# Kernel optimization log

Hardware: AMD Instinct MI355X
Metric: run time of the kernel (lower is better)

The kernel has to match this reference:

```python
import jax, jax.numpy as jnp
import numpy as np
from jax import lax

B, H, W, T = 4, 480, 640, 32
FRAME_PERIOD_US = 10000.0


def setup_inputs() -> dict:
    key = jax.random.key(0)
    k1, k2, k3 = jax.random.split(key, 3)
    # log-intensity frames, (H, W, B*T), frames of each video contiguous
    log_images = 0.25 * jax.random.normal(k1, (H, W, B * T), dtype=jnp.float32)
    video_len = jnp.full((B,), T, dtype=jnp.int64)
    image_ts = jnp.broadcast_to(jnp.arange(T, dtype=jnp.float32) * FRAME_PERIOD_US, (B, T))
    first_times = jnp.ones((B,), dtype=jnp.float32)
    # per-pixel contrast thresholds: N(mu=0.1, std=0.022), clamped to [0.01, 1.0]
    thresholds = jnp.clip(jax.random.normal(k2, (2, B, H, W), dtype=jnp.float32) * 0.022 + 0.1, 0.01, 1.0)
    log_states = jnp.zeros((B, H, W), dtype=jnp.float32)
    timestamps = jnp.zeros((B, H, W), dtype=jnp.float32)
    prev_image_ts = jnp.zeros((B,), dtype=jnp.float32)
    refractory_periods = jnp.full((B,), 100.0, dtype=jnp.float32)  # us
    leak_rates = jnp.full((B,), 0.1e-6, dtype=jnp.float32)   # per us
    shot_rates = jnp.full((B,), 1.0e-6, dtype=jnp.float32)   # per us
    threshold_mus = jnp.full((B, 2), 0.1, dtype=jnp.float32)
    rng = jax.random.uniform(k3, (T, B, H, W), dtype=jnp.float32)  # shot-noise draws
    return {
        "log_images": log_images, "video_len": video_len, "image_ts": image_ts,
        "first_times": first_times, "thresholds": thresholds, "log_states": log_states,
        "timestamps": timestamps, "prev_image_ts": prev_image_ts,
        "refractory_periods": refractory_periods, "leak_rates": leak_rates,
        "shot_rates": shot_rates, "threshold_mus": threshold_mus, "rng": rng,
    }


def reference(log_images, video_len, image_ts, first_times, thresholds, log_states,
              timestamps, prev_image_ts, refractory_periods, leak_rates, shot_rates,
              threshold_mus, rng):
    h, w = log_images.shape[:2]
    b, t = image_ts.shape
    # frames of video i are contiguous (cumsum(video_len) indexing) -> (T, B, H, W)
    frames = jnp.transpose(log_images.reshape(h, w, b, t), (3, 2, 0, 1))

    ft = first_times > 0
    ftb = ft[:, None, None]
    # on a fresh video: memorize first frame, reset last-event timestamps
    state = jnp.where(ftb, frames[0], log_states)                      # reference log level
    ts0 = jnp.where(ft, image_ts[:, 0], prev_image_ts)                 # (B,)
    last = jnp.where(ftb, (ts0 - refractory_periods)[:, None, None], timestamps)
    counts0 = jnp.zeros((b, h, w), dtype=jnp.float32)

    th_off, th_on = thresholds[0], thresholds[1]
    ref = refractory_periods[:, None, None]
    leak = leak_rates[:, None, None]
    shot = shot_rates[:, None, None]
    mu_on = threshold_mus[:, 1][:, None, None]

    def step(carry, xs):
        state, last, counts, ts_prev = carry
        frame, ts_t, u = xs
        dt = (ts_t - ts_prev)[:, None, None]
        tsb = ts_t[:, None, None]
        # leak of the reference voltage (produces ON events over time)
        state = state - leak * dt * mu_on
        diff = frame - state
        pos = diff >= 0
        th = jnp.where(pos, th_on, th_off)
        n = jnp.floor(jnp.abs(diff) / th)
        ok = ((tsb - last) >= ref).astype(n.dtype)  # refractory gating
        n = n * ok
        pol = jnp.where(pos, 1.0, -1.0)
        state = state + pol * n * th
        counts = counts + pol * n
        last = jnp.where(n > 0, tsb, last)
        # shot noise: Poisson-approx Bernoulli with p = shot_rate * dt, random polarity
        p = shot * dt
        is_shot = (u < p) & ((tsb - last) >= ref)
        pol_s = jnp.where(u < 0.5 * p, 1.0, -1.0)
        counts = counts + jnp.where(is_shot, pol_s, 0.0)
        last = jnp.where(is_shot, tsb, last)
        return (state, last, counts, ts_t), None

    xs = (frames[1:], image_ts.T[1:], rng[1:])
    (state, last, counts, _), _ = lax.scan(step, (state, last, counts0, ts0), xs)
    return counts  # signed per-pixel event counts, (B, H, W)
```

## Files before the change

kernel.cpp:

```cpp
#include <hip/hip_runtime.h>
#include <hip/hip_bf16.h>


namespace {
constexpr int Bc = 4, Hc = 480, Wc = 640, Tc = 32;
constexpr int HW  = Hc * Wc;
constexpr int BHW = Bc * HW;
}

__device__ __forceinline__ float rfl(float x) {
    return __uint_as_float(__builtin_amdgcn_readfirstlane(__float_as_uint(x)));
}

__global__ __launch_bounds__(256) void event_sim_kernel(
    const float* __restrict__ log_images,
    const float* __restrict__ image_ts,
    const float* __restrict__ first_times,
    const float* __restrict__ thresholds,
    const float* __restrict__ log_states,
    const float* __restrict__ timestamps,
    const float* __restrict__ prev_image_ts,
    const float* __restrict__ refractory,
    const float* __restrict__ leak_rates,
    const float* __restrict__ shot_rates,
    const float* __restrict__ threshold_mus,
    const float* __restrict__ rng,
    float* __restrict__ out)
{
#pragma clang fp contract(off)
    const int idx = blockIdx.x * 256 + threadIdx.x;
    if (idx >= BHW) return;
    const int b = idx / HW;
    const int p = idx - b * HW;

    const float4* fr4 = reinterpret_cast<const float4*>(log_images)
                        + ((size_t)p * Bc + b) * (Tc / 4);
    float fs[Tc];
#pragma unroll
    for (int i = 0; i < Tc / 4; ++i) {
        float4 v = fr4[i];
        fs[4*i+0] = v.x; fs[4*i+1] = v.y; fs[4*i+2] = v.z; fs[4*i+3] = v.w;
    }

    const float4* ts4 = reinterpret_cast<const float4*>(image_ts) + b * (Tc / 4);
    float tss[Tc];
#pragma unroll
    for (int i = 0; i < Tc / 4; ++i) {
        float4 v = ts4[i];
        tss[4*i+0] = rfl(v.x); tss[4*i+1] = rfl(v.y);
        tss[4*i+2] = rfl(v.z); tss[4*i+3] = rfl(v.w);
    }

    const float ref   = rfl(refractory[b]);
    const float leak  = rfl(leak_rates[b]);
    const float shot  = rfl(shot_rates[b]);
    const float mu_on = rfl(threshold_mus[2*b + 1]);
    const bool  ft    = rfl(first_times[b]) > 0.0f;
    const float pv    = rfl(prev_image_ts[b]);

    const float th_off = thresholds[idx];
    const float th_on  = thresholds[BHW + idx];

    float state   = ft ? fs[0]  : log_states[idx];
    const float ts0 = ft ? tss[0] : pv;
    float last    = ft ? (ts0 - ref) : timestamps[idx];
    float counts  = 0.0f;
    float ts_prev = ts0;

    const float* rng_base = rng + idx;

#pragma unroll
    for (int t = 1; t < Tc; ++t) {
        const float ts_t = tss[t];
        const float u    = rng_base[(size_t)t * BHW];
        const float dt   = ts_t - ts_prev;

        state = state - ((leak * dt) * mu_on);

        const float diff = fs[t] - state;
        const bool  pos  = diff >= 0.0f;
        const float th   = pos ? th_on : th_off;
        float n = floorf(fabsf(diff) / th);
        const bool okb = (ts_t - last) >= ref;
        n = okb ? n : 0.0f;
        const float pn = pos ? n : -n;
        state  = state + (pn * th);
        counts = counts + pn;
        last   = (n > 0.0f) ? ts_t : last;

        const float pshot  = shot * dt;
        const bool  is_shot = (u < pshot) && ((ts_t - last) >= ref);
        const float pol_s  = (u < (0.5f * pshot)) ? 1.0f : -1.0f;
        counts = is_shot ? (counts + pol_s) : counts;
        last   = is_shot ? ts_t : last;

        ts_prev = ts_t;
    }

    out[idx] = counts;
}

extern "C" void kernel_launch(void* const* d_in, const int* in_sizes, int n_in,
                              void* d_out, int out_size, void* d_ws, size_t ws_size,
                              hipStream_t stream) {
    const float* log_images    = (const float*)d_in[0];
    const float* image_ts      = (const float*)d_in[2];
    const float* first_times   = (const float*)d_in[3];
    const float* thresholds    = (const float*)d_in[4];
    const float* log_states    = (const float*)d_in[5];
    const float* timestamps    = (const float*)d_in[6];
    const float* prev_image_ts = (const float*)d_in[7];
    const float* refractory    = (const float*)d_in[8];
    const float* leak_rates    = (const float*)d_in[9];
    const float* shot_rates    = (const float*)d_in[10];
    const float* threshold_mus = (const float*)d_in[11];
    const float* rng           = (const float*)d_in[12];
    float* out = (float*)d_out;

    dim3 grid((BHW + 255) / 256);
    dim3 block(256);
    hipLaunchKernelGGL(event_sim_kernel, grid, block, 0, stream,
                       log_images, image_ts, first_times, thresholds,
                       log_states, timestamps, prev_image_ts, refractory,
                       leak_rates, shot_rates, threshold_mus, rng, out);
}
```

Before: 358.2 us.

## Process four pixels per thread with vectorized loads and chunked frame streaming

Each thread now handles four adjacent pixels, so thresholds, rng draws, states and outputs are read and written as 128-bit vector loads. Frames are streamed in four-timestep chunks, prefetching the next chunk instead of holding all 32 frames in registers. The intent is to cut the number of memory transactions and the register pressure, and to improve coalescing on the large rng tensor. The launch bound asks for more waves per SIMD. The grid shrinks fourfold, which lowers the thread count available to hide latency.

```diff
diff --git a/kernel.cpp b/kernel.cpp
--- a/kernel.cpp
+++ b/kernel.cpp
@@ -4,15 +4,19 @@
 
 namespace {
 constexpr int Bc = 4, Hc = 480, Wc = 640, Tc = 32;
-constexpr int HW  = Hc * Wc;
-constexpr int BHW = Bc * HW;
+constexpr int HW   = Hc * Wc;
+constexpr int BHW  = Bc * HW;
+constexpr int QHW  = HW / 4;
+constexpr int NTHR = BHW / 4;
 }
+
+typedef float v4 __attribute__((ext_vector_type(4)));
 
 __device__ __forceinline__ float rfl(float x) {
     return __uint_as_float(__builtin_amdgcn_readfirstlane(__float_as_uint(x)));
 }
 
-__global__ __launch_bounds__(256) void event_sim_kernel(
+__global__ __launch_bounds__(256, 4) void event_sim_kernel(
     const float* __restrict__ log_images,
     const float* __restrict__ image_ts,
     const float* __restrict__ first_times,
@@ -28,29 +32,19 @@
     float* __restrict__ out)
 {
 #pragma clang fp contract(off)
-    const int idx = blockIdx.x * 256 + threadIdx.x;
-    if (idx >= BHW) return;
-    const int b = idx / HW;
-    const int p = idx - b * HW;
+    const int tau = blockIdx.x * 256 + threadIdx.x;
+    const int b   = tau / QHW;
+    const int p4  = (tau - b * QHW) * 4;
+    const int base = b * HW + p4;
 
-    const float4* fr4 = reinterpret_cast<const float4*>(log_images)
-                        + ((size_t)p * Bc + b) * (Tc / 4);
-    float fs[Tc];
-#pragma unroll
-    for (int i = 0; i < Tc / 4; ++i) {
-        float4 v = fr4[i];
-        fs[4*i+0] = v.x; fs[4*i+1] = v.y; fs[4*i+2] = v.z; fs[4*i+3] = v.w;
-    }
-
-    const float4* ts4 = reinterpret_cast<const float4*>(image_ts) + b * (Tc / 4);
+    const v4* ts4p = reinterpret_cast<const v4*>(image_ts) + b * (Tc / 4);
     float tss[Tc];
 #pragma unroll
     for (int i = 0; i < Tc / 4; ++i) {
-        float4 v = ts4[i];
-        tss[4*i+0] = rfl(v.x); tss[4*i+1] = rfl(v.y);
-        tss[4*i+2] = rfl(v.z); tss[4*i+3] = rfl(v.w);
+        v4 v = ts4p[i];
+        tss[4*i+0] = rfl(v[0]); tss[4*i+1] = rfl(v[1]);
+        tss[4*i+2] = rfl(v[2]); tss[4*i+3] = rfl(v[3]);
     }
-
     const float ref   = rfl(refractory[b]);
     const float leak  = rfl(leak_rates[b]);
     const float shot  = rfl(shot_rates[b]);
@@ -58,46 +52,92 @@
     const bool  ft    = rfl(first_times[b]) > 0.0f;
     const float pv    = rfl(prev_image_ts[b]);
 
-    const float th_off = thresholds[idx];
-    const float th_on  = thresholds[BHW + idx];
+    const v4 thoff4 = *reinterpret_cast<const v4*>(thresholds + base);
+    const v4 thon4  = *reinterpret_cast<const v4*>(thresholds + BHW + base);
 
-    float state   = ft ? fs[0]  : log_states[idx];
-    const float ts0 = ft ? tss[0] : pv;
-    float last    = ft ? (ts0 - ref) : timestamps[idx];
-    float counts  = 0.0f;
+    v4 fc[4];
+#pragma unroll
+    for (int i = 0; i < 4; ++i)
+        fc[i] = *reinterpret_cast<const v4*>(log_images + (p4 + i) * (4 * Tc) + b * Tc);
+
+    float state[4], last[4], counts[4];
+    float ts0;
+    if (ft) {
+        ts0 = tss[0];
+#pragma unroll
+        for (int i = 0; i < 4; ++i) {
+            state[i] = fc[i][0];
+            last[i]  = ts0 - ref;
+        }
+    } else {
+        ts0 = pv;
+        const v4 st4 = *reinterpret_cast<const v4*>(log_states + base);
+        const v4 tm4 = *reinterpret_cast<const v4*>(timestamps + base);
+#pragma unroll
+        for (int i = 0; i < 4; ++i) { state[i] = st4[i]; last[i] = tm4[i]; }
+    }
+#pragma unroll
+    for (int i = 0; i < 4; ++i) counts[i] = 0.0f;
     float ts_prev = ts0;
 
-    const float* rng_base = rng + idx;
+#pragma unroll
+    for (int s = 0; s < 8; ++s) {
+        v4 fn[4];
+        if (s < 7) {
+#pragma unroll
+            for (int i = 0; i < 4; ++i)
+                fn[i] = *reinterpret_cast<const v4*>(
+                    log_images + (p4 + i) * (4 * Tc) + b * Tc + 4 * (s + 1));
+        }
+        v4 u4[4];
+#pragma unroll
+        for (int tt = 0; tt < 4; ++tt) {
+            const int t = 4 * s + tt;
+            if (t >= 1 && t < Tc)
+                u4[tt] = *reinterpret_cast<const v4*>(rng + t * BHW + base);
+        }
+#pragma unroll
+        for (int tt = 0; tt < 4; ++tt) {
+            const int t = 4 * s + tt;
+            if (t < 1) continue;
+            const float ts_t = tss[t];
+            const float dt   = ts_t - ts_prev;
+            const float lk   = (leak * dt) * mu_on;
+            const float psh  = shot * dt;
+#pragma unroll
+            for (int i = 0; i < 4; ++i) {
+                float st = state[i] - lk;
+                const float diff = fc[i][tt] - st;
+                const bool  pos  = diff >= 0.0f;
+                const float th   = pos ? thon4[i] : thoff4[i];
+                float n = floorf(fabsf(diff) / th);
+                const bool okb = (ts_t - last[i]) >= ref;
+                n = okb ? n : 0.0f;
+                const float pn = pos ? n : -n;
+                st = st + (pn * th);
+                float cn = counts[i] + pn;
+                float ls = (n > 0.0f) ? ts_t : last[i];
 
+                const float u = u4[tt][i];
+                const bool  is_shot = (u < psh) && ((ts_t - ls) >= ref);
+                const float pol_s   = (u < (0.5f * psh)) ? 1.0f : -1.0f;
+                cn = is_shot ? (cn + pol_s) : cn;
+                ls = is_shot ? ts_t : ls;
+
+                state[i] = st; counts[i] = cn; last[i] = ls;
+            }
+            ts_prev = ts_t;
+        }
+        if (s < 7) {
 #pragma unroll
-    for (int t = 1; t < Tc; ++t) {
-        const float ts_t = tss[t];
-        const float u    = rng_base[(size_t)t * BHW];
-        const float dt   = ts_t - ts_prev;
-
-        state = state - ((leak * dt) * mu_on);
-
-        const float diff = fs[t] - state;
-        const bool  pos  = diff >= 0.0f;
-        const float th   = pos ? th_on : th_off;
-        float n = floorf(fabsf(diff) / th);
-        const bool okb = (ts_t - last) >= ref;
-        n = okb ? n : 0.0f;
-        const float pn = pos ? n : -n;
-        state  = state + (pn * th);
-        counts = counts + pn;
-        last   = (n > 0.0f) ? ts_t : last;
-
-        const float pshot  = shot * dt;
-        const bool  is_shot = (u < pshot) && ((ts_t - last) >= ref);
-        const float pol_s  = (u < (0.5f * pshot)) ? 1.0f : -1.0f;
-        counts = is_shot ? (counts + pol_s) : counts;
-        last   = is_shot ? ts_t : last;
-
-        ts_prev = ts_t;
+            for (int i = 0; i < 4; ++i) fc[i] = fn[i];
+        }
     }
 
-    out[idx] = counts;
+    v4 o;
+#pragma unroll
+    for (int i = 0; i < 4; ++i) o[i] = counts[i];
+    *reinterpret_cast<v4*>(out + base) = o;
 }
 
 extern "C" void kernel_launch(void* const* d_in, const int* in_sizes, int n_in,
@@ -117,7 +157,7 @@
     const float* rng           = (const float*)d_in[12];
     float* out = (float*)d_out;
 
-    dim3 grid((BHW + 255) / 256);
+    dim3 grid(NTHR / 256);
     dim3 block(256);
     hipLaunchKernelGGL(event_sim_kernel, grid, block, 0, stream,
                        log_images, image_ts, first_times, thresholds,
```

After: 545.6 us. 52.3% more time.
